# Kernel optimization log

Measured on AMD Instinct MI355X. Metric: run time of the kernel, lower is better.

Reference implementation:

```python
import jax, jax.numpy as jnp
import numpy as np

VOCAB = 100000
EMBED = 128
HIDDEN = 256
N_TRIPLES = 1_000_000


def setup_inputs() -> dict:
    key = jax.random.key(0)
    ks = jax.random.split(key, 12)

    def xavier(k, fan_in, fan_out):
        limit = float(np.sqrt(6.0 / (fan_in + fan_out)))
        return jax.random.uniform(k, (fan_in, fan_out), jnp.float32, -limit, limit)

    triples = jax.random.randint(ks[0], (N_TRIPLES, 3), 0, VOCAB, dtype=jnp.int32)
    entity_table = jax.random.normal(ks[1], (VOCAB, EMBED), jnp.float32) * 0.02
    relation_table = jax.random.normal(ks[2], (VOCAB, EMBED), jnp.float32) * 0.02
    return {
        "triples": triples,
        "entity_table": entity_table,
        "relation_table": relation_table,
        "W1": xavier(ks[3], 3 * EMBED, HIDDEN), "b1": jnp.zeros((HIDDEN,), jnp.float32),
        "W2": xavier(ks[4], HIDDEN, HIDDEN),    "b2": jnp.zeros((HIDDEN,), jnp.float32),
        "W3": xavier(ks[5], HIDDEN, EMBED),     "b3": jnp.zeros((EMBED,), jnp.float32),
        "Wf1": xavier(ks[6], EMBED, HIDDEN),    "bf1": jnp.zeros((HIDDEN,), jnp.float32),
        "Wf2": xavier(ks[7], HIDDEN, EMBED),    "bf2": jnp.zeros((EMBED,), jnp.float32),
    }


def reference(triples, entity_table, relation_table,
              W1, b1, W2, b2, W3, b3, Wf1, bf1, Wf2, bf2):
    # Batched gather: [N, embed] each
    e1 = entity_table[triples[:, 0]]
    rel = relation_table[triples[:, 1]]
    e2 = entity_table[triples[:, 2]]
    x = jnp.concatenate([e1, rel, e2], axis=-1)  # [N, 3*embed]
    # graph_encoder: Linear-ReLU-Linear-ReLU-Linear
    h = jax.nn.relu(x @ W1 + b1)
    h = jax.nn.relu(h @ W2 + b2)
    enc = h @ W3 + b3                            # [N, embed]
    agg = jnp.mean(enc, axis=0)                  # [embed]
    # final_encoder: Linear-ReLU-Linear
    out = jax.nn.relu(agg @ Wf1 + bf1) @ Wf2 + bf2
    return out
```

## Files before the change

### kernel.cpp

```cpp
#include <hip/hip_runtime.h>
#include <hip/hip_bf16.h>


#define EMBED 128
#define BM 64
#define NBUCKET 128

typedef __bf16 bf16x8 __attribute__((ext_vector_type(8)));
typedef __bf16 bf16x4 __attribute__((ext_vector_type(4)));
typedef float f32x4 __attribute__((ext_vector_type(4)));

__global__ void prep_all(const float* __restrict__ W1, const float* __restrict__ W2,
                         const float* __restrict__ W3,
                         __bf16* __restrict__ W1p, __bf16* __restrict__ W2p,
                         __bf16* __restrict__ W3p, float* __restrict__ prt) {
    int idx = blockIdx.x * 256 + threadIdx.x;
    if (idx < NBUCKET * 128) prt[idx] = 0.f;
    const float* src; __bf16* dst; int K, N, e;
    if (idx < 98304)       { src = W1; dst = W1p; K = 384; N = 256; e = idx; }
    else if (idx < 163840) { src = W2; dst = W2p; K = 256; N = 256; e = idx - 98304; }
    else if (idx < 196608) { src = W3; dst = W3p; K = 256; N = 128; e = idx - 163840; }
    else return;
    int j = e & 7, l = (e >> 3) & 63, t = e >> 9;
    int KT = K >> 5;
    int kt = t % KT, mt = t / KT;
    int k  = kt * 32 + (l >> 4) * 8 + j;
    int nc = mt * 16 + (l & 15);
    dst[e] = (__bf16)src[k * N + nc];
}

__global__ __launch_bounds__(256, 3) void mlp_main(
    const int* __restrict__ triples,
    const float* __restrict__ ent, const float* __restrict__ rel,
    const __bf16* __restrict__ W1p, const float* __restrict__ b1,
    const __bf16* __restrict__ W2p, const float* __restrict__ b2,
    const __bf16* __restrict__ W3p,
    float* __restrict__ part, int n)
{
    __shared__ unsigned char lds[32768];
    unsigned char* h1s = lds;
    unsigned char* h2s = lds;

    const int tid  = threadIdx.x;
    const int wave = tid >> 6;
    const int lane = tid & 63;
    const int l15  = lane & 15;
    const int l4   = lane >> 4;
    const int s0   = blockIdx.x * BM;
    const int sp   = tid >> 4;
    const int ch   = tid & 15;

    int rows[3][4];
#pragma unroll
    for (int p = 0; p < 4; p++) {
        int g = s0 + p * 16 + sp;
        const int* t = triples + (g < n ? g : 0) * 3;
        rows[0][p] = t[0]; rows[1][p] = t[1]; rows[2][p] = t[2];
    }
    {
        float4 ga[2][4], gb[2][4];
#pragma unroll
        for (int c = 0; c < 2; c++) {
            const float* tbl = (c == 1) ? rel : ent;
#pragma unroll
            for (int p = 0; p < 4; p++) {
                const float* src = tbl + (long)rows[c][p] * EMBED + ch * 8;
                ga[c][p] = *(const float4*)src;
                gb[c][p] = *(const float4*)(src + 4);
            }
        }
#pragma unroll
        for (int c = 0; c < 2; c++)
#pragma unroll
            for (int p = 0; p < 4; p++) {
                bf16x8 w;
                w[0] = (__bf16)ga[c][p].x; w[1] = (__bf16)ga[c][p].y;
                w[2] = (__bf16)ga[c][p].z; w[3] = (__bf16)ga[c][p].w;
                w[4] = (__bf16)gb[c][p].x; w[5] = (__bf16)gb[c][p].y;
                w[6] = (__bf16)gb[c][p].z; w[7] = (__bf16)gb[c][p].w;
                int s = p * 16 + sp;
                int off = c * 16384 + ((s * 256 + ch * 16) ^ ((s & 7) << 4));
                *(bf16x8*)(lds + off) = w;
            }
    }
    __syncthreads();

    f32x4 acc[4][4];
    {
        const int fb = wave * 64;
#pragma unroll
        for (int m = 0; m < 4; m++) {
            f32x4 bias = *(const f32x4*)(b1 + fb + m * 16 + l4 * 4);
#pragma unroll
            for (int nn = 0; nn < 4; nn++) acc[m][nn] = bias;
        }
    }
    __builtin_amdgcn_s_setprio(1);
#pragma unroll
    for (int kk = 0; kk < 8; kk++) {
        bf16x8 bfr[4];
#pragma unroll
        for (int nn = 0; nn < 4; nn++) {
            int s = nn * 16 + l15;
            int off = (kk >> 2) * 16384 +
                      ((s * 256 + (kk & 3) * 64 + l4 * 16) ^ ((s & 7) << 4));
            bfr[nn] = *(const bf16x8*)(lds + off);
        }
        bf16x8 afr[4];
#pragma unroll
        for (int m = 0; m < 4; m++)
            afr[m] = *(const bf16x8*)(W1p + ((wave * 4 + m) * 12 + kk) * 512 + lane * 8);
#pragma unroll
        for (int m = 0; m < 4; m++)
#pragma unroll
            for (int nn = 0; nn < 4; nn++)
                acc[m][nn] = __builtin_amdgcn_mfma_f32_16x16x32_bf16(
                    afr[m], bfr[nn], acc[m][nn], 0, 0, 0);
    }
    __builtin_amdgcn_s_setprio(0);
    float4 g2a[4], g2b[4];
#pragma unroll
    for (int p = 0; p < 4; p++) {
        const float* src = ent + (long)rows[2][p] * EMBED + ch * 8;
        g2a[p] = *(const float4*)src;
        g2b[p] = *(const float4*)(src + 4);
    }
    __syncthreads();
#pragma unroll
    for (int p = 0; p < 4; p++) {
        bf16x8 w;
        w[0] = (__bf16)g2a[p].x; w[1] = (__bf16)g2a[p].y;
        w[2] = (__bf16)g2a[p].z; w[3] = (__bf16)g2a[p].w;
        w[4] = (__bf16)g2b[p].x; w[5] = (__bf16)g2b[p].y;
        w[6] = (__bf16)g2b[p].z; w[7] = (__bf16)g2b[p].w;
        int s = p * 16 + sp;
        int off = (s * 256 + ch * 16) ^ ((s & 7) << 4);
        *(bf16x8*)(lds + off) = w;
    }
    __syncthreads();
    __builtin_amdgcn_s_setprio(1);
#pragma unroll
    for (int kk = 8; kk < 12; kk++) {
        bf16x8 bfr[4];
#pragma unroll
        for (int nn = 0; nn < 4; nn++) {
            int s = nn * 16 + l15;
            int off = (s * 256 + (kk & 3) * 64 + l4 * 16) ^ ((s & 7) << 4);
            bfr[nn] = *(const bf16x8*)(lds + off);
        }
        bf16x8 afr[4];
#pragma unroll
        for (int m = 0; m < 4; m++)
            afr[m] = *(const bf16x8*)(W1p + ((wave * 4 + m) * 12 + kk) * 512 + lane * 8);
#pragma unroll
        for (int m = 0; m < 4; m++)
#pragma unroll
            for (int nn = 0; nn < 4; nn++)
                acc[m][nn] = __builtin_amdgcn_mfma_f32_16x16x32_bf16(
                    afr[m], bfr[nn], acc[m][nn], 0, 0, 0);
    }
    __builtin_amdgcn_s_setprio(0);
    __syncthreads();
#pragma unroll
    for (int m = 0; m < 4; m++) {
        int f0 = wave * 64 + m * 16 + l4 * 4;
#pragma unroll
        for (int nn = 0; nn < 4; nn++) {
            int s = nn * 16 + l15;
            bf16x4 p;
#pragma unroll
            for (int j = 0; j < 4; j++) {
                float v = acc[m][nn][j];
                p[j] = (__bf16)(v > 0.f ? v : 0.f);
            }
            int off = (s * 512 + f0 * 2) ^ ((s & 7) << 4);
            *(bf16x4*)(h1s + off) = p;
        }
    }
    __syncthreads();

    f32x4 acc2[4][4];
    {
        const int fb = wave * 64;
#pragma unroll
        for (int m = 0; m < 4; m++) {
            f32x4 bias = *(const f32x4*)(b2 + fb + m * 16 + l4 * 4);
#pragma unroll
            for (int nn = 0; nn < 4; nn++) acc2[m][nn] = bias;
        }
    }
    __builtin_amdgcn_s_setprio(1);
#pragma unroll
    for (int kk = 0; kk < 8; kk++) {
        bf16x8 bfr[4];
#pragma unroll
        for (int nn = 0; nn < 4; nn++) {
            int s = nn * 16 + l15;
            int off = (s * 512 + kk * 64 + l4 * 16) ^ ((s & 7) << 4);
            bfr[nn] = *(const bf16x8*)(h1s + off);
        }
        bf16x8 afr[4];
#pragma unroll
        for (int m = 0; m < 4; m++)
            afr[m] = *(const bf16x8*)(W2p + ((wave * 4 + m) * 8 + kk) * 512 + lane * 8);
#pragma unroll
        for (int m = 0; m < 4; m++)
#pragma unroll
            for (int nn = 0; nn < 4; nn++)
                acc2[m][nn] = __builtin_amdgcn_mfma_f32_16x16x32_bf16(
                    afr[m], bfr[nn], acc2[m][nn], 0, 0, 0);
    }
    __builtin_amdgcn_s_setprio(0);
    __syncthreads();
#pragma unroll
    for (int m = 0; m < 4; m++) {
        int f0 = wave * 64 + m * 16 + l4 * 4;
#pragma unroll
        for (int nn = 0; nn < 4; nn++) {
            int s = nn * 16 + l15;
            bf16x4 p;
#pragma unroll
            for (int j = 0; j < 4; j++) {
                float v = acc2[m][nn][j];
                p[j] = (__bf16)(v > 0.f ? v : 0.f);
            }
            int off = (s * 512 + f0 * 2) ^ ((s & 7) << 4);
            *(bf16x4*)(h2s + off) = p;
        }
    }
    __syncthreads();

    f32x4 acc3[2][4];
#pragma unroll
    for (int m = 0; m < 2; m++)
#pragma unroll
        for (int nn = 0; nn < 4; nn++)
            acc3[m][nn] = (f32x4)(0.f);
    __builtin_amdgcn_s_setprio(1);
#pragma unroll
    for (int kk = 0; kk < 8; kk++) {
        bf16x8 bfr[4];
#pragma unroll
        for (int nn = 0; nn < 4; nn++) {
            int s = nn * 16 + l15;
            int off = (s * 512 + kk * 64 + l4 * 16) ^ ((s & 7) << 4);
            bfr[nn] = *(const bf16x8*)(h2s + off);
        }
        bf16x8 afr[2];
#pragma unroll
        for (int m = 0; m < 2; m++)
            afr[m] = *(const bf16x8*)(W3p + ((wave * 2 + m) * 8 + kk) * 512 + lane * 8);
#pragma unroll
        for (int m = 0; m < 2; m++)
#pragma unroll
            for (int nn = 0; nn < 4; nn++)
                acc3[m][nn] = __builtin_amdgcn_mfma_f32_16x16x32_bf16(
                    afr[m], bfr[nn], acc3[m][nn], 0, 0, 0);
    }
    __builtin_amdgcn_s_setprio(0);
    {
        float* bucket = part + (blockIdx.x & (NBUCKET - 1)) * 128;
#pragma unroll
        for (int m = 0; m < 2; m++) {
#pragma unroll
            for (int j = 0; j < 4; j++) {
                float v = 0.f;
#pragma unroll
                for (int nn = 0; nn < 4; nn++) {
                    int g = s0 + nn * 16 + l15;
                    float t = acc3[m][nn][j];
                    v += (g < n) ? t : 0.f;
                }
                for (int off = 1; off < 16; off <<= 1) v += __shfl_xor(v, off);
                if (l15 == 0) {
                    int f = wave * 32 + m * 16 + l4 * 4 + j;
                    atomicAdd(bucket + f, v);
                }
            }
        }
    }
}

__global__ void head_kernel(const float* __restrict__ part, const float* __restrict__ b3,
                            const float* __restrict__ Wf1, const float* __restrict__ bf1,
                            const float* __restrict__ Wf2, const float* __restrict__ bf2,
                            float* __restrict__ out, int n)
{
    __shared__ float agg[128];
    __shared__ float t[256];
    const int tid = threadIdx.x;
    if (tid < 128) {
        float s = 0.f;
        for (int b = 0; b < NBUCKET; b++) s += part[b * 128 + tid];
        agg[tid] = s / (float)n + b3[tid];
    }
    __syncthreads();
    {
        float a = bf1[tid];
        for (int k = 0; k < 128; k++) a += agg[k] * Wf1[k * 256 + tid];
        t[tid] = a > 0.f ? a : 0.f;
    }
    __syncthreads();
    if (tid < 128) {
        float o = bf2[tid];
        for (int i = 0; i < 256; i++) o += t[i] * Wf2[i * 128 + tid];
        out[tid] = o;
    }
}

extern "C" void kernel_launch(void* const* d_in, const int* in_sizes, int n_in,
                              void* d_out, int out_size, void* d_ws, size_t ws_size,
                              hipStream_t stream) {
    const int*   triples = (const int*)d_in[0];
    const float* ent     = (const float*)d_in[1];
    const float* rel     = (const float*)d_in[2];
    const float* W1      = (const float*)d_in[3];
    const float* b1      = (const float*)d_in[4];
    const float* W2      = (const float*)d_in[5];
    const float* b2      = (const float*)d_in[6];
    const float* W3      = (const float*)d_in[7];
    const float* b3      = (const float*)d_in[8];
    const float* Wf1     = (const float*)d_in[9];
    const float* bf1     = (const float*)d_in[10];
    const float* Wf2     = (const float*)d_in[11];
    const float* bf2     = (const float*)d_in[12];
    float* out = (float*)d_out;
    const int n = in_sizes[0] / 3;

    __bf16* W1p = (__bf16*)d_ws;
    __bf16* W2p = (__bf16*)((char*)d_ws + 196608);
    __bf16* W3p = (__bf16*)((char*)d_ws + 327680);
    float*  prt = (float*)((char*)d_ws + 393216);

    prep_all<<<768, 256, 0, stream>>>(W1, W2, W3, W1p, W2p, W3p, prt);

    const int blocks = (n + BM - 1) / BM;
    mlp_main<<<blocks, 256, 0, stream>>>(triples, ent, rel, W1p, b1, W2p, b2, W3p, prt, n);
    head_kernel<<<1, 256, 0, stream>>>(prt, b3, Wf1, bf1, Wf2, bf2, out, n);
}
```

Before: 542.0 us.

## Precompute per-vocab first-layer projections and gather them instead of embeddings

Splits the first linear layer by linearity: each vocab row's entity and relation embeddings are multiplied by the matching W1 slices once (100k rows, three tables), and the main kernel gathers and sums three 256-wide bf16 projections per triple instead of doing the 384x256 matmul. This removes the largest GEMM from the 1M-row path, at the cost of a precompute pass over the vocabulary and larger bf16 gathers (three 512-byte rows per triple instead of three 512-byte fp32 rows). It depends on having enough workspace. Otherwise a fallback kernel gathers all three embeddings at once into a larger LDS buffer. Rounding the projections to bf16 before the add adds some precision risk.

```diff
diff --git a/kernel.cpp b/kernel.cpp
--- a/kernel.cpp
+++ b/kernel.cpp
@@ -5,6 +5,7 @@
 #define EMBED 128
 #define BM 64
 #define NBUCKET 128
+#define VOCAB 100000
 
 typedef __bf16 bf16x8 __attribute__((ext_vector_type(8)));
 typedef __bf16 bf16x4 __attribute__((ext_vector_type(4)));
@@ -29,7 +30,251 @@
     dst[e] = (__bf16)src[k * N + nc];
 }
 
-__global__ __launch_bounds__(256, 3) void mlp_main(
+__global__ __launch_bounds__(256, 2) void precompute_P(
+    const float* __restrict__ ent, const float* __restrict__ rel,
+    const __bf16* __restrict__ W1p,
+    __bf16* __restrict__ Pa, __bf16* __restrict__ Pb, __bf16* __restrict__ Pc)
+{
+    __shared__ unsigned char xs[32768];
+    const int tid  = threadIdx.x;
+    const int wave = tid >> 6;
+    const int lane = tid & 63;
+    const int l15  = lane & 15;
+    const int l4   = lane >> 4;
+    const int v0   = blockIdx.x * 64;
+    const int sp   = tid >> 4;
+    const int ch   = tid & 15;
+
+#pragma unroll
+    for (int p = 0; p < 4; p++) {
+        int vr = p * 16 + sp;
+        int v  = v0 + vr;
+        int vc = v < VOCAB ? v : 0;
+        const float* se = ent + (long)vc * EMBED + ch * 8;
+        const float* sr = rel + (long)vc * EMBED + ch * 8;
+        float4 e0 = *(const float4*)se, e1 = *(const float4*)(se + 4);
+        float4 r0 = *(const float4*)sr, r1 = *(const float4*)(sr + 4);
+        bf16x8 we, wr;
+        we[0] = (__bf16)e0.x; we[1] = (__bf16)e0.y; we[2] = (__bf16)e0.z; we[3] = (__bf16)e0.w;
+        we[4] = (__bf16)e1.x; we[5] = (__bf16)e1.y; we[6] = (__bf16)e1.z; we[7] = (__bf16)e1.w;
+        wr[0] = (__bf16)r0.x; wr[1] = (__bf16)r0.y; wr[2] = (__bf16)r0.z; wr[3] = (__bf16)r0.w;
+        wr[4] = (__bf16)r1.x; wr[5] = (__bf16)r1.y; wr[6] = (__bf16)r1.z; wr[7] = (__bf16)r1.w;
+        int swz = (vr & 7) << 4;
+        *(bf16x8*)(xs + ((vr * 512 + ch * 16) ^ swz))       = we;
+        *(bf16x8*)(xs + ((vr * 512 + 256 + ch * 16) ^ swz)) = wr;
+    }
+    __syncthreads();
+
+    __bf16* const outs[3] = {Pa, Pb, Pc};
+#pragma unroll
+    for (int ph = 0; ph < 3; ph++) {
+        const int breg = (ph == 1) ? 256 : 0;
+        f32x4 acc[4][4];
+#pragma unroll
+        for (int m = 0; m < 4; m++)
+#pragma unroll
+            for (int nn = 0; nn < 4; nn++) acc[m][nn] = (f32x4)(0.f);
+#pragma unroll
+        for (int kk = 0; kk < 4; kk++) {
+            bf16x8 bfr[4];
+#pragma unroll
+            for (int nn = 0; nn < 4; nn++) {
+                int s = nn * 16 + l15;
+                int off = (s * 512 + breg + kk * 64 + l4 * 16) ^ ((s & 7) << 4);
+                bfr[nn] = *(const bf16x8*)(xs + off);
+            }
+            bf16x8 afr[4];
+#pragma unroll
+            for (int m = 0; m < 4; m++)
+                afr[m] = *(const bf16x8*)(W1p + ((wave * 4 + m) * 12 + ph * 4 + kk) * 512 + lane * 8);
+#pragma unroll
+            for (int m = 0; m < 4; m++)
+#pragma unroll
+                for (int nn = 0; nn < 4; nn++)
+                    acc[m][nn] = __builtin_amdgcn_mfma_f32_16x16x32_bf16(
+                        afr[m], bfr[nn], acc[m][nn], 0, 0, 0);
+        }
+        __bf16* out = outs[ph];
+#pragma unroll
+        for (int m = 0; m < 4; m++)
+#pragma unroll
+            for (int nn = 0; nn < 4; nn++) {
+                int v = v0 + nn * 16 + l15;
+                if (v < VOCAB) {
+                    int f = wave * 64 + m * 16 + l4 * 4;
+                    bf16x4 pk;
+#pragma unroll
+                    for (int j = 0; j < 4; j++) pk[j] = (__bf16)acc[m][nn][j];
+                    *(bf16x4*)(out + (long)v * 256 + f) = pk;
+                }
+            }
+    }
+}
+
+__global__ __launch_bounds__(256, 3) void mlp_mainP(
+    const int* __restrict__ triples,
+    const __bf16* __restrict__ Pa, const __bf16* __restrict__ Pb,
+    const __bf16* __restrict__ Pc, const float* __restrict__ b1,
+    const __bf16* __restrict__ W2p, const float* __restrict__ b2,
+    const __bf16* __restrict__ W3p,
+    float* __restrict__ part, int n)
+{
+    __shared__ unsigned char lds[32768];
+    unsigned char* h1s = lds;
+    unsigned char* h2s = lds;
+
+    const int tid  = threadIdx.x;
+    const int wave = tid >> 6;
+    const int lane = tid & 63;
+    const int l15  = lane & 15;
+    const int l4   = lane >> 4;
+    const int s0   = blockIdx.x * BM;
+
+    {
+        const int s = tid >> 2;
+        const int q = tid & 3;
+        int g = s0 + s;
+        const int* tp = triples + (long)(g < n ? g : 0) * 3;
+        const uint4* ra = (const uint4*)(Pa + (long)tp[0] * 256 + q * 64);
+        const uint4* rb = (const uint4*)(Pb + (long)tp[1] * 256 + q * 64);
+        const uint4* rc = (const uint4*)(Pc + (long)tp[2] * 256 + q * 64);
+        uint4 va[8], vb[8], vc[8];
+#pragma unroll
+        for (int i = 0; i < 8; i++) { va[i] = ra[i]; vb[i] = rb[i]; vc[i] = rc[i]; }
+        const float* bp = b1 + q * 64;
+        const int swz = (s & 7) << 4;
+#pragma unroll
+        for (int i = 0; i < 8; i++) {
+            bf16x8 a = *reinterpret_cast<const bf16x8*>(&va[i]);
+            bf16x8 b = *reinterpret_cast<const bf16x8*>(&vb[i]);
+            bf16x8 c = *reinterpret_cast<const bf16x8*>(&vc[i]);
+            f32x4 b0 = *(const f32x4*)(bp + i * 8);
+            f32x4 b1v = *(const f32x4*)(bp + i * 8 + 4);
+            bf16x8 r;
+#pragma unroll
+            for (int j = 0; j < 4; j++) {
+                float v = (float)a[j] + (float)b[j] + (float)c[j] + b0[j];
+                r[j] = (__bf16)(v > 0.f ? v : 0.f);
+            }
+#pragma unroll
+            for (int j = 0; j < 4; j++) {
+                float v = (float)a[4 + j] + (float)b[4 + j] + (float)c[4 + j] + b1v[j];
+                r[4 + j] = (__bf16)(v > 0.f ? v : 0.f);
+            }
+            int off = (s * 512 + q * 128 + i * 16) ^ swz;
+            *(bf16x8*)(h1s + off) = r;
+        }
+    }
+    __syncthreads();
+
+    f32x4 acc2[2][4];
+    f32x4 acc2b[2][4];
+    {
+        const int fb = wave * 64;
+#pragma unroll
+        for (int m = 0; m < 2; m++) {
+            f32x4 bias = *(const f32x4*)(b2 + fb + m * 16 + l4 * 4);
+            f32x4 biasb = *(const f32x4*)(b2 + fb + (m + 2) * 16 + l4 * 4);
+#pragma unroll
+            for (int nn = 0; nn < 4; nn++) { acc2[m][nn] = bias; acc2b[m][nn] = biasb; }
+        }
+    }
+    __builtin_amdgcn_s_setprio(1);
+#pragma unroll
+    for (int kk = 0; kk < 8; kk++) {
+        bf16x8 bfr[4];
+#pragma unroll
+        for (int nn = 0; nn < 4; nn++) {
+            int s = nn * 16 + l15;
+            int off = (s * 512 + kk * 64 + l4 * 16) ^ ((s & 7) << 4);
+            bfr[nn] = *(const bf16x8*)(h1s + off);
+        }
+        bf16x8 afr[4];
+#pragma unroll
+        for (int m = 0; m < 4; m++)
+            afr[m] = *(const bf16x8*)(W2p + ((wave * 4 + m) * 8 + kk) * 512 + lane * 8);
+#pragma unroll
+        for (int m = 0; m < 2; m++)
+#pragma unroll
+            for (int nn = 0; nn < 4; nn++) {
+                acc2[m][nn] = __builtin_amdgcn_mfma_f32_16x16x32_bf16(
+                    afr[m], bfr[nn], acc2[m][nn], 0, 0, 0);
+                acc2b[m][nn] = __builtin_amdgcn_mfma_f32_16x16x32_bf16(
+                    afr[m + 2], bfr[nn], acc2b[m][nn], 0, 0, 0);
+            }
+    }
+    __builtin_amdgcn_s_setprio(0);
+    __syncthreads();
+#pragma unroll
+    for (int m = 0; m < 4; m++) {
+        int f0 = wave * 64 + m * 16 + l4 * 4;
+#pragma unroll
+        for (int nn = 0; nn < 4; nn++) {
+            int s = nn * 16 + l15;
+            bf16x4 p;
+#pragma unroll
+            for (int j = 0; j < 4; j++) {
+                float v = (m < 2) ? acc2[m][nn][j] : acc2b[m - 2][nn][j];
+                p[j] = (__bf16)(v > 0.f ? v : 0.f);
+            }
+            int off = (s * 512 + f0 * 2) ^ ((s & 7) << 4);
+            *(bf16x4*)(h2s + off) = p;
+        }
+    }
+    __syncthreads();
+
+    f32x4 acc3[2][4];
+#pragma unroll
+    for (int m = 0; m < 2; m++)
+#pragma unroll
+        for (int nn = 0; nn < 4; nn++)
+            acc3[m][nn] = (f32x4)(0.f);
+    __builtin_amdgcn_s_setprio(1);
+#pragma unroll
+    for (int kk = 0; kk < 8; kk++) {
+        bf16x8 bfr[4];
+#pragma unroll
+        for (int nn = 0; nn < 4; nn++) {
+            int s = nn * 16 + l15;
+            int off = (s * 512 + kk * 64 + l4 * 16) ^ ((s & 7) << 4);
+            bfr[nn] = *(const bf16x8*)(h2s + off);
+        }
+        bf16x8 afr[2];
+#pragma unroll
+        for (int m = 0; m < 2; m++)
+            afr[m] = *(const bf16x8*)(W3p + ((wave * 2 + m) * 8 + kk) * 512 + lane * 8);
+#pragma unroll
+        for (int m = 0; m < 2; m++)
+#pragma unroll
+            for (int nn = 0; nn < 4; nn++)
+                acc3[m][nn] = __builtin_amdgcn_mfma_f32_16x16x32_bf16(
+                    afr[m], bfr[nn], acc3[m][nn], 0, 0, 0);
+    }
+    __builtin_amdgcn_s_setprio(0);
+    {
+        float* bucket = part + (blockIdx.x & (NBUCKET - 1)) * 128;
+#pragma unroll
+        for (int m = 0; m < 2; m++) {
+#pragma unroll
+            for (int j = 0; j < 4; j++) {
+                float v = 0.f;
+#pragma unroll
+                for (int nn = 0; nn < 4; nn++) {
+                    int g = s0 + nn * 16 + l15;
+                    float t = acc3[m][nn][j];
+                    v += (g < n) ? t : 0.f;
+                }
+                for (int off = 1; off < 16; off <<= 1) v += __shfl_xor(v, off);
+                if (l15 == 0) {
+                    int f = wave * 32 + m * 16 + l4 * 4 + j;
+                    atomicAdd(bucket + f, v);
+                }
+            }
+        }
+    }
+}
+
+__global__ __launch_bounds__(256, 3) void mlp_main_r4(
     const int* __restrict__ triples,
     const float* __restrict__ ent, const float* __restrict__ rel,
     const __bf16* __restrict__ W1p, const float* __restrict__ b1,
@@ -37,10 +282,10 @@
     const __bf16* __restrict__ W3p,
     float* __restrict__ part, int n)
 {
-    __shared__ unsigned char lds[32768];
+    __shared__ unsigned char lds[49152];
+    unsigned char* xs  = lds;
     unsigned char* h1s = lds;
     unsigned char* h2s = lds;
-
     const int tid  = threadIdx.x;
     const int wave = tid >> 6;
     const int lane = tid & 63;
@@ -57,32 +302,30 @@
         const int* t = triples + (g < n ? g : 0) * 3;
         rows[0][p] = t[0]; rows[1][p] = t[1]; rows[2][p] = t[2];
     }
-    {
-        float4 ga[2][4], gb[2][4];
-#pragma unroll
-        for (int c = 0; c < 2; c++) {
-            const float* tbl = (c == 1) ? rel : ent;
-#pragma unroll
-            for (int p = 0; p < 4; p++) {
-                const float* src = tbl + (long)rows[c][p] * EMBED + ch * 8;
-                ga[c][p] = *(const float4*)src;
-                gb[c][p] = *(const float4*)(src + 4);
-            }
-        }
-#pragma unroll
-        for (int c = 0; c < 2; c++)
-#pragma unroll
-            for (int p = 0; p < 4; p++) {
-                bf16x8 w;
-                w[0] = (__bf16)ga[c][p].x; w[1] = (__bf16)ga[c][p].y;
-                w[2] = (__bf16)ga[c][p].z; w[3] = (__bf16)ga[c][p].w;
-                w[4] = (__bf16)gb[c][p].x; w[5] = (__bf16)gb[c][p].y;
-                w[6] = (__bf16)gb[c][p].z; w[7] = (__bf16)gb[c][p].w;
-                int s = p * 16 + sp;
-                int off = c * 16384 + ((s * 256 + ch * 16) ^ ((s & 7) << 4));
-                *(bf16x8*)(lds + off) = w;
-            }
-    }
+    float4 ga[3][4], gb[3][4];
+#pragma unroll
+    for (int c = 0; c < 3; c++) {
+        const float* tbl = (c == 1) ? rel : ent;
+#pragma unroll
+        for (int p = 0; p < 4; p++) {
+            const float* src = tbl + (long)rows[c][p] * EMBED + ch * 8;
+            ga[c][p] = *(const float4*)src;
+            gb[c][p] = *(const float4*)(src + 4);
+        }
+    }
+#pragma unroll
+    for (int c = 0; c < 3; c++)
+#pragma unroll
+        for (int p = 0; p < 4; p++) {
+            bf16x8 w;
+            w[0] = (__bf16)ga[c][p].x; w[1] = (__bf16)ga[c][p].y;
+            w[2] = (__bf16)ga[c][p].z; w[3] = (__bf16)ga[c][p].w;
+            w[4] = (__bf16)gb[c][p].x; w[5] = (__bf16)gb[c][p].y;
+            w[6] = (__bf16)gb[c][p].z; w[7] = (__bf16)gb[c][p].w;
+            int s = p * 16 + sp;
+            int off = (s * 768 + c * 256 + ch * 16) ^ ((s & 7) << 4);
+            *(bf16x8*)(xs + off) = w;
+        }
     __syncthreads();
 
     f32x4 acc[4][4];
@@ -97,56 +340,13 @@
     }
     __builtin_amdgcn_s_setprio(1);
 #pragma unroll
-    for (int kk = 0; kk < 8; kk++) {
+    for (int kk = 0; kk < 12; kk++) {
         bf16x8 bfr[4];
 #pragma unroll
         for (int nn = 0; nn < 4; nn++) {
             int s = nn * 16 + l15;
-            int off = (kk >> 2) * 16384 +
-                      ((s * 256 + (kk & 3) * 64 + l4 * 16) ^ ((s & 7) << 4));
-            bfr[nn] = *(const bf16x8*)(lds + off);
-        }
-        bf16x8 afr[4];
-#pragma unroll
-        for (int m = 0; m < 4; m++)
-            afr[m] = *(const bf16x8*)(W1p + ((wave * 4 + m) * 12 + kk) * 512 + lane * 8);
-#pragma unroll
-        for (int m = 0; m < 4; m++)
-#pragma unroll
-            for (int nn = 0; nn < 4; nn++)
-                acc[m][nn] = __builtin_amdgcn_mfma_f32_16x16x32_bf16(
-                    afr[m], bfr[nn], acc[m][nn], 0, 0, 0);
-    }
-    __builtin_amdgcn_s_setprio(0);
-    float4 g2a[4], g2b[4];
-#pragma unroll
-    for (int p = 0; p < 4; p++) {
-        const float* src = ent + (long)rows[2][p] * EMBED + ch * 8;
-        g2a[p] = *(const float4*)src;
-        g2b[p] = *(const float4*)(src + 4);
-    }
-    __syncthreads();
-#pragma unroll
-    for (int p = 0; p < 4; p++) {
-        bf16x8 w;
-        w[0] = (__bf16)g2a[p].x; w[1] = (__bf16)g2a[p].y;
-        w[2] = (__bf16)g2a[p].z; w[3] = (__bf16)g2a[p].w;
-        w[4] = (__bf16)g2b[p].x; w[5] = (__bf16)g2b[p].y;
-        w[6] = (__bf16)g2b[p].z; w[7] = (__bf16)g2b[p].w;
-        int s = p * 16 + sp;
-        int off = (s * 256 + ch * 16) ^ ((s & 7) << 4);
-        *(bf16x8*)(lds + off) = w;
-    }
-    __syncthreads();
-    __builtin_amdgcn_s_setprio(1);
-#pragma unroll
-    for (int kk = 8; kk < 12; kk++) {
-        bf16x8 bfr[4];
-#pragma unroll
-        for (int nn = 0; nn < 4; nn++) {
-            int s = nn * 16 + l15;
-            int off = (s * 256 + (kk & 3) * 64 + l4 * 16) ^ ((s & 7) << 4);
-            bfr[nn] = *(const bf16x8*)(lds + off);
+            int off = (s * 768 + kk * 64 + l4 * 16) ^ ((s & 7) << 4);
+            bfr[nn] = *(const bf16x8*)(xs + off);
         }
         bf16x8 afr[4];
 #pragma unroll
@@ -331,10 +531,21 @@
     __bf16* W2p = (__bf16*)((char*)d_ws + 196608);
     __bf16* W3p = (__bf16*)((char*)d_ws + 327680);
     float*  prt = (float*)((char*)d_ws + 393216);
+    const size_t P_OFF = 458752;
+    const size_t P_ELEMS = (size_t)VOCAB * 256;
+    const size_t NEED = P_OFF + 3 * P_ELEMS * sizeof(__bf16);
 
     prep_all<<<768, 256, 0, stream>>>(W1, W2, W3, W1p, W2p, W3p, prt);
 
     const int blocks = (n + BM - 1) / BM;
-    mlp_main<<<blocks, 256, 0, stream>>>(triples, ent, rel, W1p, b1, W2p, b2, W3p, prt, n);
+    if (ws_size >= NEED) {
+        __bf16* Pa = (__bf16*)((char*)d_ws + P_OFF);
+        __bf16* Pb = Pa + P_ELEMS;
+        __bf16* Pc = Pb + P_ELEMS;
+        precompute_P<<<(VOCAB + 63) / 64, 256, 0, stream>>>(ent, rel, W1p, Pa, Pb, Pc);
+        mlp_mainP<<<blocks, 256, 0, stream>>>(triples, Pa, Pb, Pc, b1, W2p, b2, W3p, prt, n);
+    } else {
+        mlp_main_r4<<<blocks, 256, 0, stream>>>(triples, ent, rel, W1p, b1, W2p, b2, W3p, prt, n);
+    }
     head_kernel<<<1, 256, 0, stream>>>(prt, b3, Wf1, bf1, Wf2, bf2, out, n);
 }
```

Result: slower. 618.7 us (+14.1%).
